# Kernel optimization log

Hardware: AMD Instinct MI355X
Metric: run time of the kernel (lower is better)

## Reference

```python
import jax, jax.numpy as jnp
import numpy as np

L, D, OC, GROUPS, EPS = 256, 1280, 128, 8, 1e-5


def setup_inputs() -> dict:
    key = jax.random.key(0)
    k1, k2 = jax.random.split(key)
    feats = jax.random.normal(k1, (L, D), dtype=jnp.float32)
    # Conv2d(3d, out_ch, kernel_size=1) weight flattened to (out_ch, 3d)
    W = jax.random.normal(k2, (OC, 3 * D), dtype=jnp.float32) * (1.0 / np.sqrt(3 * D))
    b = jnp.zeros((OC,), dtype=jnp.float32)
    gamma = jnp.ones((OC,), dtype=jnp.float32)
    beta = jnp.zeros((OC,), dtype=jnp.float32)
    return {"feats": feats, "W": W, "b": b, "gamma": gamma, "beta": beta}


def reference(feats, W, b, gamma, beta):
    fi = feats[:, None, :]                     # (L, 1, d)
    fj = feats[None, :, :]                     # (1, L, d)
    add = fi + fj                              # (L, L, d)
    diff = jnp.abs(fi - fj)                    # (L, L, d)
    had = fi * fj                              # (L, L, d)
    pair = jnp.concatenate([add, diff, had], axis=-1)  # (L, L, 3d)
    # 1x1 conv == per-pixel linear: (L, L, 3d) x (out_ch, 3d)^T -> (L, L, out_ch)
    x = jnp.einsum('ijc,oc->ijo', pair, W) + b
    # GroupNorm(8, out_ch) on batch=1: normalize over (C/g, L, L) per group
    xg = jnp.transpose(x, (2, 0, 1)).reshape(GROUPS, OC // GROUPS, L, L)
    mean = jnp.mean(xg, axis=(1, 2, 3), keepdims=True)
    var = jnp.var(xg, axis=(1, 2, 3), keepdims=True)
    xn = ((xg - mean) * jax.lax.rsqrt(var + EPS)).reshape(OC, L, L)
    xn = xn * gamma[:, None, None] + beta[:, None, None]
    out = jax.nn.gelu(xn, approximate=False)   # torch nn.GELU default = exact erf
    return out[None]                           # (1, out_ch, L, L)
```

## Files before the change

kernel.cpp:

```cpp
#include <hip/hip_runtime.h>
#include <math.h>

typedef unsigned int uint;
typedef unsigned short ushort;

typedef __attribute__((ext_vector_type(8))) __bf16 bf16x8;
typedef __attribute__((ext_vector_type(16))) float floatx16;

#define NFEAT 327680
#define NW    491520

union U4B8 { uint4 u; bf16x8 b; };

__device__ inline ushort f2b(float f) {
  uint u = __float_as_uint(f);
  u += 0x7fffu + ((u >> 16) & 1u);
  return (ushort)(u >> 16);
}
__device__ inline float blo(uint u) { return __uint_as_float(u << 16); }
__device__ inline float bhi(uint u) { return __uint_as_float(u & 0xffff0000u); }

#if __has_builtin(__builtin_amdgcn_cvt_pk_bf16_f32)
typedef __attribute__((ext_vector_type(2))) __bf16 bf16x2;
__device__ inline uint cvtpk(float a, float b) {
  bf16x2 r = __builtin_amdgcn_cvt_pk_bf16_f32(a, b);
  return *(uint*)&r;
}
__device__ inline uint cvtpk_abs(float a, float b) { return cvtpk(fabsf(a), fabsf(b)); }
#else
__device__ inline uint cvtpk(float a, float b) {
  uint au = __float_as_uint(a) + 0x8000u;
  uint bu = __float_as_uint(b) + 0x8000u;
  return __builtin_amdgcn_perm(bu, au, 0x07060302u);
}
__device__ inline uint cvtpk_abs(float a, float b) { return cvtpk(a, b) & 0x7fff7fffu; }
#endif

__device__ inline void async16(const ushort* g, ushort* l) {
  __builtin_amdgcn_global_load_lds((const __attribute__((address_space(1))) uint*)g,
                                   (__attribute__((address_space(3))) uint*)l, 16, 0, 0);
}

__global__ void prep_kernel(const float* __restrict__ feats,
                            const float* __restrict__ W,
                            ushort* __restrict__ fB,
                            ushort* __restrict__ wB,
                            float* __restrict__ stats,
                            float* __restrict__ Aoi) {
  int idx = blockIdx.x * 256 + threadIdx.x;
  if (blockIdx.x == 0 && threadIdx.x < 16) stats[threadIdx.x] = 0.0f;
  if (idx < 32768) Aoi[idx] = 0.0f;
  if (idx < NFEAT) fB[idx] = f2b(feats[idx]);
  else             wB[idx - NFEAT] = f2b(W[idx - NFEAT]);
}

__global__ __launch_bounds__(256, 2) void gemma_kernel(
    const ushort* __restrict__ fB, const ushort* __restrict__ wB,
    float* __restrict__ Aoi) {
  __shared__ float red[4][4096];
  const int tid = threadIdx.x, lane = tid & 63, w = tid >> 6;
  const int i0 = (blockIdx.x >> 2) << 5;
  const int kq = blockIdx.x & 3;
  const int rr = lane & 31, half = lane >> 5;
  floatx16 a4[4];
  #pragma unroll
  for (int ot = 0; ot < 4; ++ot)
    #pragma unroll
    for (int r = 0; r < 16; ++r) a4[ot][r] = 0.0f;
  const int kbase = kq * 320 + w * 80 + half * 8;
  #pragma unroll
  for (int ks = 0; ks < 5; ++ks) {
    const int k = kbase + ks * 16;
    U4B8 bf; bf.u = *(const uint4*)(fB + (i0 + rr) * 1280 + k);
    #pragma unroll
    for (int ot = 0; ot < 4; ++ot) {
      U4B8 af; af.u = *(const uint4*)(wB + (ot * 32 + rr) * 3840 + k);
      a4[ot] = __builtin_amdgcn_mfma_f32_32x32x16_bf16(af.b, bf.b, a4[ot], 0, 0, 0);
    }
  }
  #pragma unroll
  for (int ot = 0; ot < 4; ++ot)
    #pragma unroll
    for (int r = 0; r < 16; ++r) {
      const int orow = (r & 3) + 8 * (r >> 2) + 4 * half;
      red[w][(ot * 32 + orow) * 32 + rr] = a4[ot][r];
    }
  __syncthreads();
  for (int e = tid; e < 4096; e += 256) {
    float s = red[0][e] + red[1][e] + red[2][e] + red[3][e];
    atomicAdd(&Aoi[(e >> 5) * 256 + i0 + (e & 31)], s);
  }
}

__device__ inline void build(const uint4 vj, const float fi8[8], U4B8& d, U4B8& h) {
  uint ju[4] = {vj.x, vj.y, vj.z, vj.w};
  uint* pd = &d.u.x; uint* ph = &h.u.x;
  #pragma unroll
  for (int t = 0; t < 4; ++t) {
    float j0f = blo(ju[t]), j1f = bhi(ju[t]);
    float i0 = fi8[2 * t], i1 = fi8[2 * t + 1];
    pd[t] = cvtpk_abs(i0 - j0f, i1 - j1f);
    ph[t] = cvtpk(i0 * j0f, i1 * j1f);
  }
}

__global__ __launch_bounds__(256, 5) void gemm_kernel(
    const ushort* __restrict__ fB, const ushort* __restrict__ wB,
    const float* __restrict__ bias, const float* __restrict__ Aoi,
    float* __restrict__ xout, float* __restrict__ stats) {
  __shared__ __align__(16) ushort Wl[2 * 128 * 64];

  const int tid = threadIdx.x;
  const int blk = blockIdx.x;
  const int i_row = blk >> 2;
  const int j0 = (blk & 3) << 6;
  const int lane = tid & 63;
  const int w = tid >> 6;
  const int wo = (w >> 1) << 6;
  const int wm = (w & 1) << 5;
  const int rr = lane & 31;
  const int half = lane >> 5;
  const int rr7 = lane & 7;

  const ushort* gsrc[4];
  #pragma unroll
  for (int p = 0; p < 4; ++p) {
    const int seg = w * 4 + p;
    const int row = seg * 8 + (lane >> 3);
    const int g = (lane & 7) ^ (lane >> 3);
    gsrc[p] = wB + row * 3840 + 1280 + (g >> 2) * 1280 + (g & 3) * 8;
  }

  const ushort* fip = fB + i_row * 1280 + half * 8;
  const ushort* fjp = fB + (j0 + wm + rr) * 1280 + half * 8;

  floatx16 acc[2];
  #pragma unroll
  for (int a = 0; a < 2; ++a)
    #pragma unroll
    for (int r = 0; r < 16; ++r) acc[a][r] = 0.0f;

  #pragma unroll
  for (int p = 0; p < 4; ++p)
    async16(gsrc[p], &Wl[(w * 4 + p) * 512]);
  uint4 vi[2], vj[2];
  #pragma unroll
  for (int st = 0; st < 2; ++st) {
    vi[st] = *(const uint4*)(fip + st * 16);
    vj[st] = *(const uint4*)(fjp + st * 16);
  }
  __syncthreads();

  for (int cc = 0; cc < 40; ++cc) {
    const ushort* Wc = &Wl[(cc & 1) * 8192];
    uint4 vin[2], vjn[2];
    if (cc < 39) {
      const int cn = (cc + 1) << 5;
      #pragma unroll
      for (int p = 0; p < 4; ++p)
        async16(gsrc[p] + cn, &Wl[((cc & 1) ^ 1) * 8192 + (w * 4 + p) * 512]);
      __builtin_amdgcn_sched_barrier(0);
      #pragma unroll
      for (int st = 0; st < 2; ++st) {
        vin[st] = *(const uint4*)(fip + cn + st * 16);
        vjn[st] = *(const uint4*)(fjp + cn + st * 16);
      }
      __builtin_amdgcn_sched_barrier(0);
    }
    #pragma unroll
    for (int st = 0; st < 2; ++st) {
      float fi8[8];
      {
        uint iu[4] = {vi[st].x, vi[st].y, vi[st].z, vi[st].w};
        #pragma unroll
        for (int t = 0; t < 4; ++t) { fi8[2*t] = blo(iu[t]); fi8[2*t+1] = bhi(iu[t]); }
      }
      U4B8 dfr, hfr;
      build(vj[st], fi8, dfr, hfr);
      const int g0 = (st << 1) + half;
      #pragma unroll
      for (int ot = 0; ot < 2; ++ot) {
        const int rowb = (wo + ot * 32 + rr) << 6;
        bf16x8 ad = *(const bf16x8*)(Wc + rowb + ((g0 ^ rr7) << 3));
        bf16x8 ah = *(const bf16x8*)(Wc + rowb + (((g0 + 4) ^ rr7) << 3));
        acc[ot] = __builtin_amdgcn_mfma_f32_32x32x16_bf16(ad, dfr.b, acc[ot], 0, 0, 0);
        acc[ot] = __builtin_amdgcn_mfma_f32_32x32x16_bf16(ah, hfr.b, acc[ot], 0, 0, 0);
      }
    }
    if (cc < 39) {
      __builtin_amdgcn_sched_barrier(0);
      __builtin_amdgcn_s_waitcnt(0x0F74);
      __builtin_amdgcn_s_barrier();
      __builtin_amdgcn_sched_barrier(0);
      __asm__ volatile("" ::: "memory");
      #pragma unroll
      for (int st = 0; st < 2; ++st) { vi[st] = vin[st]; vj[st] = vjn[st]; }
    }
  }

  float gs[2][2] = {{0.f, 0.f}, {0.f, 0.f}};
  float gq[2][2] = {{0.f, 0.f}, {0.f, 0.f}};
  const int jg = j0 + wm + rr;
  const int mglob = i_row * 256 + jg;
  #pragma unroll
  for (int ot = 0; ot < 2; ++ot) {
    #pragma unroll
    for (int r = 0; r < 16; ++r) {
      const int orow = (r & 3) + 8 * (r >> 2) + 4 * half;
      const int o = wo + ot * 32 + orow;
      float x = acc[ot][r] + Aoi[o * 256 + i_row] + Aoi[o * 256 + jg] + bias[o];
      xout[o * 65536 + mglob] = x;
      gs[ot][r >> 3] += x;
      gq[ot][r >> 3] += x * x;
    }
  }
  __syncthreads();
  float* sred = (float*)Wl;
  if (tid < 16) sred[tid] = 0.0f;
  __syncthreads();
  #pragma unroll
  for (int ot = 0; ot < 2; ++ot) {
    #pragma unroll
    for (int rg = 0; rg < 2; ++rg) {
      float s = gs[ot][rg], qv = gq[ot][rg];
      for (int off = 32; off > 0; off >>= 1) {
        s += __shfl_xor(s, off, 64);
        qv += __shfl_xor(qv, off, 64);
      }
      if (lane == 0) {
        const int g = (wo >> 4) + ot * 2 + rg;
        atomicAdd(&sred[g], s);
        atomicAdd(&sred[8 + g], qv);
      }
    }
  }
  __syncthreads();
  if (tid < 16) atomicAdd(&stats[tid], sred[tid]);
}

__global__ void norm_kernel(float* __restrict__ xout,
                            const float* __restrict__ stats,
                            const float* __restrict__ gamma,
                            const float* __restrict__ beta) {
  const int idx = blockIdx.x * 256 + threadIdx.x;
  const int e = idx << 2;
  const int o = e >> 16;
  const int g = o >> 4;
  const float invN = 1.0f / 1048576.0f;
  const float mean = stats[g] * invN;
  const float var = stats[8 + g] * invN - mean * mean;
  const float inv = rsqrtf(var + 1e-5f);
  const float ga = gamma[o], be = beta[o];
  float4 v = *(float4*)(xout + e);
  float* pv = &v.x;
  #pragma unroll
  for (int t = 0; t < 4; ++t) {
    float xn = (pv[t] - mean) * inv * ga + be;
    pv[t] = 0.5f * xn * (1.0f + erff(xn * 0.70710678118654752f));
  }
  *(float4*)(xout + e) = v;
}

extern "C" void kernel_launch(void* const* d_in, const int* in_sizes, int n_in,
                              void* d_out, int out_size, void* d_ws, size_t ws_size,
                              hipStream_t stream) {
  const float* feats = (const float*)d_in[0];
  const float* W     = (const float*)d_in[1];
  const float* bias  = (const float*)d_in[2];
  const float* gamma = (const float*)d_in[3];
  const float* beta  = (const float*)d_in[4];
  float* out = (float*)d_out;

  ushort* fB = (ushort*)d_ws;
  ushort* wB = fB + NFEAT;
  float* stats = (float*)(wB + NW);
  float* Aoi = stats + 16;

  prep_kernel<<<3200, 256, 0, stream>>>(feats, W, fB, wB, stats, Aoi);
  gemma_kernel<<<32, 256, 0, stream>>>(fB, wB, Aoi);
  gemm_kernel<<<1024, 256, 0, stream>>>(fB, wB, bias, Aoi, out, stats);
  norm_kernel<<<8192, 256, 0, stream>>>(out, stats, gamma, beta);
}
```

Measured before the change: 180.1 us.

## Process two i-rows per gemm block to reuse W tiles; split gemma over output tiles

The main GEMM block now computes two i rows against the same 64 j columns. Each staged W tile in shared memory and each j fragment feeds twice as many MFMAs, and the grid halves to 512 blocks with launch bounds lowered to 2. The small Aoi GEMM is spread over 128 blocks, one output tile each, instead of 32, to add parallelism. The cost is a larger accumulator and register footprint, which lowers occupancy, and fewer blocks to hide latency. The waitcnt is adjusted for the extra outstanding loads.

```diff
diff --git a/kernel.cpp b/kernel.cpp
--- a/kernel.cpp
+++ b/kernel.cpp
@@ -6,6 +6,7 @@
 
 typedef __attribute__((ext_vector_type(8))) __bf16 bf16x8;
 typedef __attribute__((ext_vector_type(16))) float floatx16;
+typedef __attribute__((ext_vector_type(2))) float f32x2;
 
 #define NFEAT 327680
 #define NW    491520
@@ -17,8 +18,12 @@
   u += 0x7fffu + ((u >> 16) & 1u);
   return (ushort)(u >> 16);
 }
-__device__ inline float blo(uint u) { return __uint_as_float(u << 16); }
-__device__ inline float bhi(uint u) { return __uint_as_float(u & 0xffff0000u); }
+__device__ inline f32x2 unpk(uint u) {
+  f32x2 r;
+  r.x = __uint_as_float(u << 16);
+  r.y = __uint_as_float(u & 0xffff0000u);
+  return r;
+}
 
 #if __has_builtin(__builtin_amdgcn_cvt_pk_bf16_f32)
 typedef __attribute__((ext_vector_type(2))) __bf16 bf16x2;
@@ -57,54 +62,51 @@
 __global__ __launch_bounds__(256, 2) void gemma_kernel(
     const ushort* __restrict__ fB, const ushort* __restrict__ wB,
     float* __restrict__ Aoi) {
-  __shared__ float red[4][4096];
+  __shared__ float red[4][1024];
   const int tid = threadIdx.x, lane = tid & 63, w = tid >> 6;
-  const int i0 = (blockIdx.x >> 2) << 5;
-  const int kq = blockIdx.x & 3;
+  const int i0 = (blockIdx.x >> 4) << 5;
+  const int kq = (blockIdx.x >> 2) & 3;
+  const int ot = blockIdx.x & 3;
   const int rr = lane & 31, half = lane >> 5;
-  floatx16 a4[4];
-  #pragma unroll
-  for (int ot = 0; ot < 4; ++ot)
-    #pragma unroll
-    for (int r = 0; r < 16; ++r) a4[ot][r] = 0.0f;
+  floatx16 a4;
+  #pragma unroll
+  for (int r = 0; r < 16; ++r) a4[r] = 0.0f;
   const int kbase = kq * 320 + w * 80 + half * 8;
   #pragma unroll
   for (int ks = 0; ks < 5; ++ks) {
     const int k = kbase + ks * 16;
     U4B8 bf; bf.u = *(const uint4*)(fB + (i0 + rr) * 1280 + k);
-    #pragma unroll
-    for (int ot = 0; ot < 4; ++ot) {
-      U4B8 af; af.u = *(const uint4*)(wB + (ot * 32 + rr) * 3840 + k);
-      a4[ot] = __builtin_amdgcn_mfma_f32_32x32x16_bf16(af.b, bf.b, a4[ot], 0, 0, 0);
-    }
-  }
-  #pragma unroll
-  for (int ot = 0; ot < 4; ++ot)
-    #pragma unroll
-    for (int r = 0; r < 16; ++r) {
-      const int orow = (r & 3) + 8 * (r >> 2) + 4 * half;
-      red[w][(ot * 32 + orow) * 32 + rr] = a4[ot][r];
-    }
-  __syncthreads();
-  for (int e = tid; e < 4096; e += 256) {
+    U4B8 af; af.u = *(const uint4*)(wB + (ot * 32 + rr) * 3840 + k);
+    a4 = __builtin_amdgcn_mfma_f32_32x32x16_bf16(af.b, bf.b, a4, 0, 0, 0);
+  }
+  #pragma unroll
+  for (int r = 0; r < 16; ++r) {
+    const int orow = (r & 3) + 8 * (r >> 2) + 4 * half;
+    red[w][orow * 32 + rr] = a4[r];
+  }
+  __syncthreads();
+  for (int e = tid; e < 1024; e += 256) {
     float s = red[0][e] + red[1][e] + red[2][e] + red[3][e];
-    atomicAdd(&Aoi[(e >> 5) * 256 + i0 + (e & 31)], s);
-  }
-}
-
-__device__ inline void build(const uint4 vj, const float fi8[8], U4B8& d, U4B8& h) {
-  uint ju[4] = {vj.x, vj.y, vj.z, vj.w};
-  uint* pd = &d.u.x; uint* ph = &h.u.x;
+    atomicAdd(&Aoi[(ot * 32 + (e >> 5)) * 256 + i0 + (e & 31)], s);
+  }
+}
+
+__device__ inline void build_pair(const f32x2 jv[4], const uint4 vi, U4B8& d, U4B8& h) {
+  uint iu[4] = {vi.x, vi.y, vi.z, vi.w};
+  uint du[4], hu[4];
   #pragma unroll
   for (int t = 0; t < 4; ++t) {
-    float j0f = blo(ju[t]), j1f = bhi(ju[t]);
-    float i0 = fi8[2 * t], i1 = fi8[2 * t + 1];
-    pd[t] = cvtpk_abs(i0 - j0f, i1 - j1f);
-    ph[t] = cvtpk(i0 * j0f, i1 * j1f);
-  }
-}
-
-__global__ __launch_bounds__(256, 5) void gemm_kernel(
+    f32x2 fv = unpk(iu[t]);
+    f32x2 dd = fv - jv[t];
+    f32x2 hh = fv * jv[t];
+    du[t] = cvtpk_abs(dd.x, dd.y);
+    hu[t] = cvtpk(hh.x, hh.y);
+  }
+  d.u = make_uint4(du[0], du[1], du[2], du[3]);
+  h.u = make_uint4(hu[0], hu[1], hu[2], hu[3]);
+}
+
+__global__ __launch_bounds__(256, 2) void gemm_kernel(
     const ushort* __restrict__ fB, const ushort* __restrict__ wB,
     const float* __restrict__ bias, const float* __restrict__ Aoi,
     float* __restrict__ xout, float* __restrict__ stats) {
@@ -112,7 +114,7 @@
 
   const int tid = threadIdx.x;
   const int blk = blockIdx.x;
-  const int i_row = blk >> 2;
+  const int i0 = (blk >> 2) << 1;
   const int j0 = (blk & 3) << 6;
   const int lane = tid & 63;
   const int w = tid >> 6;
@@ -131,29 +133,33 @@
     gsrc[p] = wB + row * 3840 + 1280 + (g >> 2) * 1280 + (g & 3) * 8;
   }
 
-  const ushort* fip = fB + i_row * 1280 + half * 8;
+  const ushort* fi0p = fB + i0 * 1280 + half * 8;
+  const ushort* fi1p = fi0p + 1280;
   const ushort* fjp = fB + (j0 + wm + rr) * 1280 + half * 8;
 
-  floatx16 acc[2];
+  floatx16 acc[2][2];
   #pragma unroll
   for (int a = 0; a < 2; ++a)
     #pragma unroll
-    for (int r = 0; r < 16; ++r) acc[a][r] = 0.0f;
+    for (int ot = 0; ot < 2; ++ot)
+      #pragma unroll
+      for (int r = 0; r < 16; ++r) acc[a][ot][r] = 0.0f;
 
   #pragma unroll
   for (int p = 0; p < 4; ++p)
     async16(gsrc[p], &Wl[(w * 4 + p) * 512]);
-  uint4 vi[2], vj[2];
+  uint4 vi0[2], vi1[2], vj[2];
   #pragma unroll
   for (int st = 0; st < 2; ++st) {
-    vi[st] = *(const uint4*)(fip + st * 16);
-    vj[st] = *(const uint4*)(fjp + st * 16);
+    vj[st]  = *(const uint4*)(fjp  + st * 16);
+    vi0[st] = *(const uint4*)(fi0p + st * 16);
+    vi1[st] = *(const uint4*)(fi1p + st * 16);
   }
   __syncthreads();
 
   for (int cc = 0; cc < 40; ++cc) {
     const ushort* Wc = &Wl[(cc & 1) * 8192];
-    uint4 vin[2], vjn[2];
+    uint4 vi0n[2], vi1n[2], vjn[2];
     if (cc < 39) {
       const int cn = (cc + 1) << 5;
       #pragma unroll
@@ -162,56 +168,66 @@
       __builtin_amdgcn_sched_barrier(0);
       #pragma unroll
       for (int st = 0; st < 2; ++st) {
-        vin[st] = *(const uint4*)(fip + cn + st * 16);
-        vjn[st] = *(const uint4*)(fjp + cn + st * 16);
+        vjn[st]  = *(const uint4*)(fjp  + cn + st * 16);
+        vi0n[st] = *(const uint4*)(fi0p + cn + st * 16);
+        vi1n[st] = *(const uint4*)(fi1p + cn + st * 16);
       }
       __builtin_amdgcn_sched_barrier(0);
     }
     #pragma unroll
     for (int st = 0; st < 2; ++st) {
-      float fi8[8];
+      f32x2 jv[4];
       {
-        uint iu[4] = {vi[st].x, vi[st].y, vi[st].z, vi[st].w};
+        uint ju[4] = {vj[st].x, vj[st].y, vj[st].z, vj[st].w};
         #pragma unroll
-        for (int t = 0; t < 4; ++t) { fi8[2*t] = blo(iu[t]); fi8[2*t+1] = bhi(iu[t]); }
-      }
-      U4B8 dfr, hfr;
-      build(vj[st], fi8, dfr, hfr);
+        for (int t = 0; t < 4; ++t) jv[t] = unpk(ju[t]);
+      }
+      U4B8 d0, h0, d1, h1;
+      build_pair(jv, vi0[st], d0, h0);
+      build_pair(jv, vi1[st], d1, h1);
       const int g0 = (st << 1) + half;
       #pragma unroll
       for (int ot = 0; ot < 2; ++ot) {
         const int rowb = (wo + ot * 32 + rr) << 6;
         bf16x8 ad = *(const bf16x8*)(Wc + rowb + ((g0 ^ rr7) << 3));
         bf16x8 ah = *(const bf16x8*)(Wc + rowb + (((g0 + 4) ^ rr7) << 3));
-        acc[ot] = __builtin_amdgcn_mfma_f32_32x32x16_bf16(ad, dfr.b, acc[ot], 0, 0, 0);
-        acc[ot] = __builtin_amdgcn_mfma_f32_32x32x16_bf16(ah, hfr.b, acc[ot], 0, 0, 0);
+        acc[0][ot] = __builtin_amdgcn_mfma_f32_32x32x16_bf16(ad, d0.b, acc[0][ot], 0, 0, 0);
+        acc[1][ot] = __builtin_amdgcn_mfma_f32_32x32x16_bf16(ad, d1.b, acc[1][ot], 0, 0, 0);
+        acc[0][ot] = __builtin_amdgcn_mfma_f32_32x32x16_bf16(ah, h0.b, acc[0][ot], 0, 0, 0);
+        acc[1][ot] = __builtin_amdgcn_mfma_f32_32x32x16_bf16(ah, h1.b, acc[1][ot], 0, 0, 0);
       }
     }
     if (cc < 39) {
       __builtin_amdgcn_sched_barrier(0);
-      __builtin_amdgcn_s_waitcnt(0x0F74);
+      __builtin_amdgcn_s_waitcnt(0x0F76);
       __builtin_amdgcn_s_barrier();
       __builtin_amdgcn_sched_barrier(0);
       __asm__ volatile("" ::: "memory");
       #pragma unroll
-      for (int st = 0; st < 2; ++st) { vi[st] = vin[st]; vj[st] = vjn[st]; }
+      for (int st = 0; st < 2; ++st) {
+        vj[st] = vjn[st]; vi0[st] = vi0n[st]; vi1[st] = vi1n[st];
+      }
     }
   }
 
   float gs[2][2] = {{0.f, 0.f}, {0.f, 0.f}};
   float gq[2][2] = {{0.f, 0.f}, {0.f, 0.f}};
   const int jg = j0 + wm + rr;
-  const int mglob = i_row * 256 + jg;
-  #pragma unroll
-  for (int ot = 0; ot < 2; ++ot) {
-    #pragma unroll
-    for (int r = 0; r < 16; ++r) {
-      const int orow = (r & 3) + 8 * (r >> 2) + 4 * half;
-      const int o = wo + ot * 32 + orow;
-      float x = acc[ot][r] + Aoi[o * 256 + i_row] + Aoi[o * 256 + jg] + bias[o];
-      xout[o * 65536 + mglob] = x;
-      gs[ot][r >> 3] += x;
-      gq[ot][r >> 3] += x * x;
+  #pragma unroll
+  for (int ii = 0; ii < 2; ++ii) {
+    const int irow = i0 + ii;
+    const int mglob = irow * 256 + jg;
+    #pragma unroll
+    for (int ot = 0; ot < 2; ++ot) {
+      #pragma unroll
+      for (int r = 0; r < 16; ++r) {
+        const int orow = (r & 3) + 8 * (r >> 2) + 4 * half;
+        const int o = wo + ot * 32 + orow;
+        float x = acc[ii][ot][r] + Aoi[o * 256 + irow] + Aoi[o * 256 + jg] + bias[o];
+        xout[o * 65536 + mglob] = x;
+        gs[ot][r >> 3] += x;
+        gq[ot][r >> 3] += x * x;
+      }
     }
   }
   __syncthreads();
@@ -277,7 +293,7 @@
   float* Aoi = stats + 16;
 
   prep_kernel<<<3200, 256, 0, stream>>>(feats, W, fB, wB, stats, Aoi);
-  gemma_kernel<<<32, 256, 0, stream>>>(fB, wB, Aoi);
-  gemm_kernel<<<1024, 256, 0, stream>>>(fB, wB, bias, Aoi, out, stats);
+  gemma_kernel<<<128, 256, 0, stream>>>(fB, wB, Aoi);
+  gemm_kernel<<<512, 256, 0, stream>>>(fB, wB, bias, Aoi, out, stats);
   norm_kernel<<<8192, 256, 0, stream>>>(out, stats, gamma, beta);
 }
```

New measurement: 154.1 us. -14.4%, faster.
